# Kernel tuning notes

Measured on AMD Instinct MI355X. Metric: run time of the kernel, lower is better.

Reference implementation:

```python
import jax, jax.numpy as jnp
import numpy as np

B, T, N, H = 16, 49, 24, 256
S = 0.05  # init scale (keeps sigmoids/tanh out of saturation for numeric testing)


def setup_inputs() -> dict:
    key = jax.random.key(0)
    ks = jax.random.split(key, 16)
    rn = lambda k, shp: (jax.random.normal(k, shp, dtype=jnp.float32) * S)
    return dict(
        h=rn(ks[0], (B, T, N, H)),
        c_h=rn(ks[1], (B, T, N, H)),
        p=rn(ks[2], (B, T, N, H)),
        g_t=rn(ks[3], (B, T, N, H)),
        c_g_t=rn(ks[4], (B, T, N, H)),
        g_s=rn(ks[5], (B, T, N, H)),
        c_g_s=rn(ks[6], (B, T, N, H)),
        # 9 h-gates stacked in order: i, lt, ft, rt, s, gt, gs, o, c
        U=rn(ks[7], (9, N, H, H)),
        Wt=rn(ks[8], (9, N, 3 * H, H)),
        Ws=rn(ks[9], (9, N, H, H)),
        Zt=rn(ks[10], (9, N, H, H)),
        Zs=rn(ks[11], (9, N, H, H)),
        b=rn(ks[12], (9, N, 1, H)),
        # 6 global gates stacked in order: gtf, gtg, gto, gsf, gsg, gso
        Wg=rn(ks[13], (6, N, H, H)),
        Zg=rn(ks[14], (6, N, H, H)),
        bg=rn(ks[15], (6, N, 1, H)),
        train=1,
    )


def _cell(h, c_h, p, g_t, c_g_t, g_s, c_g_s, U, Wt, Ws, Zt, Zs, b, Wg, Zg, bg):
    pad_t = jnp.zeros_like(h[:, :, :1, :])
    pad_s = jnp.zeros_like(h[:, :1, :, :])
    # spatial (bone) neighbours along axis 2
    h_t_before = jnp.concatenate([pad_t, h[:, :, :-1, :]], axis=2)
    h_t_after = jnp.concatenate([h[:, :, 1:, :], pad_t], axis=2)
    h_tba = jnp.concatenate([h_t_before, h, h_t_after], axis=3)  # [B,T,N,3H]
    c_t_before = jnp.concatenate([pad_t, c_h[:, :, :-1, :]], axis=2)
    c_t_after = jnp.concatenate([c_h[:, :, 1:, :], pad_t], axis=2)
    # temporal predecessor along axis 1
    h_s_before = jnp.concatenate([pad_s, h[:, :-1, :, :]], axis=1)
    c_s_before = jnp.concatenate([pad_s, c_h[:, :-1, :, :]], axis=1)

    # Faithful quirk of the source: f_ft gate uses Zslt (the lt gate's Zs) for its g_s term.
    Zs_eff = Zs.at[2].set(Zs[1])

    # All 9 gate preactivations in one fused batched-GEMM pass: [9,B,T,N,H]
    pre = (jnp.einsum('btnh,gnhk->gbtnk', p, U)
           + jnp.einsum('btnm,gnmk->gbtnk', h_tba, Wt)
           + jnp.einsum('btnh,gnhk->gbtnk', h_s_before, Ws)
           + jnp.einsum('btnh,gnhk->gbtnk', g_t, Zt)
           + jnp.einsum('btnh,gnhk->gbtnk', g_s, Zs_eff)
           + b[:, None, None, :, 0, :])
    i_n, f_lt, f_ft, f_rt, f_s, f_gt, f_gs, o_n = jax.nn.sigmoid(pre[:8])
    c_n = jnp.tanh(pre[8])

    c_h_new = (f_lt * c_t_before + f_ft * c_h + f_rt * c_t_after
               + f_s * c_s_before + f_gt * c_g_t + f_gs * c_g_s + i_n * c_n)
    h_new = o_n * jnp.tanh(c_h_new)

    def _global(x_g, c_g, Wg3, Zg3, bg3):
        pre_g = (jnp.einsum('btnh,gnhk->gbtnk', h_new, Wg3)
                 + jnp.einsum('btnh,gnhk->gbtnk', x_g, Zg3)
                 + bg3[:, None, None, :, 0, :])
        f_g = jax.nn.sigmoid(pre_g[0])
        cand = jnp.tanh(pre_g[1])
        o_g = jax.nn.sigmoid(pre_g[2])
        c_g_new = f_g * c_g + (1.0 - f_g) * cand
        return o_g * jnp.tanh(c_g_new), c_g_new

    g_t_new, c_g_t_new = _global(g_t, c_g_t, Wg[:3], Zg[:3], bg[:3])
    g_s_new, c_g_s_new = _global(g_s, c_g_s, Wg[3:], Zg[3:], bg[3:])
    return h_new, c_h_new, g_t_new, c_g_t_new, g_s_new, c_g_s_new


def reference(h, c_h, p, g_t, c_g_t, g_s, c_g_s, U, Wt, Ws, Zt, Zs, b, Wg, Zg, bg, train):
    # `train` is a flag unused by the cell's math (kept for signature fidelity)
    return _cell(h, c_h, p, g_t, c_g_t, g_s, c_g_s, U, Wt, Ws, Zt, Zs, b, Wg, Zg, bg)
```

## Files before the change

kernel.cpp:

```cpp
#include <hip/hip_runtime.h>
#include <hip/hip_bf16.h>

typedef unsigned short u16;
typedef u16 u16x8 __attribute__((ext_vector_type(8)));
typedef short s16x8 __attribute__((ext_vector_type(8)));
typedef float f32x4 __attribute__((ext_vector_type(4)));
typedef unsigned int u32;

#define NN 24
#define TT 49
#define MR 784
#define SZT 4816896

__device__ inline u16 f2b(float f){
    __hip_bfloat16 b = __float2bfloat16(f); u16 r; __builtin_memcpy(&r, &b, 2); return r;
}
__device__ inline float sig_(float x){ return 1.f / (1.f + __expf(-x)); }
__device__ inline float tanh_(float x){ float e = __expf(2.f * x); return (e - 1.f) / (e + 1.f); }

__device__ inline void gld16(const u16* g, u16* l){
    __builtin_amdgcn_global_load_lds(
        (const __attribute__((address_space(1))) unsigned int*)g,
        (__attribute__((address_space(3))) unsigned int*)l, 16, 0, 0);
}

#define BAR()      __builtin_amdgcn_s_barrier()
#define WAITVM(N)  asm volatile("s_waitcnt vmcnt(" #N ")" ::: "memory")
#define WAITVL(N)  asm volatile("s_waitcnt vmcnt(" #N ") lgkmcnt(0)" ::: "memory")

#define WT0_ELEMS ((size_t)216 * 256 * 1792)
#define WT1_ELEMS ((size_t)144 * 256 * 512)

__global__ __launch_bounds__(256) void prep_all(
    const float* __restrict__ U,  const float* __restrict__ Wt,
    const float* __restrict__ Ws, const float* __restrict__ Zt,
    const float* __restrict__ Zs, const float* __restrict__ Wg,
    const float* __restrict__ Zg,
    const float* __restrict__ p,  const float* __restrict__ h,
    const float* __restrict__ g_t, const float* __restrict__ g_s,
    u16* __restrict__ wt0, u16* __restrict__ wt1, u16* __restrict__ Abf)
{
    __shared__ u16 T[64][72];
    const int tid = threadIdx.x;
    const int lin = blockIdx.x;

    if (lin < 24192) {
        const int kt = lin % 28, ct = (lin / 28) % 4, z = lin / 112;
        const int n = z % NN, g = z / NN;
        const int k0 = kt * 64;
        const float* wbase;
        if (k0 < 256)       wbase = U  + (size_t)((g * NN + n) * 256 + k0)          * 256;
        else if (k0 < 1024) wbase = Wt + (size_t)((g * NN + n) * 768 + (k0 - 256))  * 256;
        else if (k0 < 1280) wbase = Ws + (size_t)((g * NN + n) * 256 + (k0 - 1024)) * 256;
        else if (k0 < 1536) wbase = Zt + (size_t)((g * NN + n) * 256 + (k0 - 1280)) * 256;
        else { const int g2 = (g == 2) ? 1 : g;
               wbase = Zs + (size_t)((g2 * NN + n) * 256 + (k0 - 1536)) * 256; }
        const int colg = ct * 64 + (tid & 15) * 4;
        #pragma unroll
        for (int it = 0; it < 4; ++it) {
            const int krl = (tid >> 4) + it * 16;
            const float4 v = *(const float4*)(wbase + (size_t)krl * 256 + colg);
            const int cl = (tid & 15) * 4;
            T[cl + 0][krl] = f2b(v.x); T[cl + 1][krl] = f2b(v.y);
            T[cl + 2][krl] = f2b(v.z); T[cl + 3][krl] = f2b(v.w);
        }
        __syncthreads();
        const int col_l = tid >> 2, ks = (tid & 3) * 16;
        const int ktile = 2 * kt + (ks >> 5);
        const int koff  = ks & 31;
        u16* dst = wt0 + (size_t)z * 458752 + (size_t)ktile * 8192
                       + (size_t)(ct * 64 + col_l) * 32 + koff;
        u16x8 w0, w1;
        #pragma unroll
        for (int j2 = 0; j2 < 8; ++j2) { w0[j2] = T[col_l][ks + j2]; w1[j2] = T[col_l][ks + 8 + j2]; }
        *(u16x8*)(dst) = w0; *(u16x8*)(dst + 8) = w1;
    } else if (lin < 28800) {
        const int l = lin - 24192;
        const int kt = l % 8, ct = (l / 8) % 4, z = l / 32;
        const int k0 = kt * 64;
        const float* wbase = (k0 < 256)
            ? Wg + (size_t)(z * 256 + k0) * 256
            : Zg + (size_t)(z * 256 + (k0 - 256)) * 256;
        const int colg = ct * 64 + (tid & 15) * 4;
        #pragma unroll
        for (int it = 0; it < 4; ++it) {
            const int krl = (tid >> 4) + it * 16;
            const float4 v = *(const float4*)(wbase + (size_t)krl * 256 + colg);
            const int cl = (tid & 15) * 4;
            T[cl + 0][krl] = f2b(v.x); T[cl + 1][krl] = f2b(v.y);
            T[cl + 2][krl] = f2b(v.z); T[cl + 3][krl] = f2b(v.w);
        }
        __syncthreads();
        const int col_l = tid >> 2, ks = (tid & 3) * 16;
        const int ktile = 2 * kt + (ks >> 5);
        const int koff  = ks & 31;
        u16* dst = wt1 + (size_t)z * 131072 + (size_t)ktile * 8192
                       + (size_t)(ct * 64 + col_l) * 32 + koff;
        u16x8 w0, w1;
        #pragma unroll
        for (int j2 = 0; j2 < 8; ++j2) { w0[j2] = T[col_l][ks + j2]; w1[j2] = T[col_l][ks + 8 + j2]; }
        *(u16x8*)(dst) = w0; *(u16x8*)(dst + 8) = w1;
    } else {
        const int l = lin - 28800;
        const int bx = l % 13, kt = (l / 13) % 56, n = l / 728;
        const int row = bx * 64 + (tid >> 2);
        if (row >= MR) return;
        const int c  = tid & 3;
        const int kg = kt * 32 + c * 8;
        const int seg = kg >> 8, koff = kg & 255;
        const int ec = (row * NN + n) * 256 + koff;
        const float* src = nullptr; bool valid = true;
        switch (seg) {
            case 0: src = p + ec; break;
            case 1: valid = (n > 0);          src = h + ec - 256; break;
            case 2: src = h + ec; break;
            case 3: valid = (n < NN - 1);     src = h + ec + 256; break;
            case 4: valid = (row % TT) != 0;  src = h + ec - NN * 256; break;
            case 5: src = g_t + ec; break;
            default: src = g_s + ec; break;
        }
        float4 lo = {0.f,0.f,0.f,0.f}, hi = lo;
        if (valid) { lo = *(const float4*)src; hi = *(const float4*)(src + 4); }
        u16x8 w;
        w[0] = f2b(lo.x); w[1] = f2b(lo.y); w[2] = f2b(lo.z); w[3] = f2b(lo.w);
        w[4] = f2b(hi.x); w[5] = f2b(hi.y); w[6] = f2b(hi.z); w[7] = f2b(hi.w);
        *(u16x8*)(Abf + ((size_t)(n * 56 + kt) * MR + row) * 32 + c * 8) = w;
    }
}

#define AB8 4096
#define BB8 18432

__global__ __launch_bounds__(512, 1) void fused_cell8(
    const float* __restrict__ c_h, const float* __restrict__ c_g_t,
    const float* __restrict__ c_g_s,
    const u16* __restrict__ Abf, const u16* __restrict__ WT0,
    const float* __restrict__ Bias,
    float* __restrict__ h_new, float* __restrict__ c_h_new)
{
    extern __shared__ u16 smem[];

    const int tid = threadIdx.x;
    const int lin = blockIdx.x;
    const int xcd = lin & 7, j = lin >> 3;
    const int mtile = j % 7;
    const int slab  = (j / 7) * 8 + xcd;
    const int ntile = slab & 3, n = slab >> 2;

    const int wave = tid >> 6, lane = tid & 63;
    const int rh = wave >> 2, cq = wave & 3;
    const int lrow = lane & 15, lci = lane >> 4;

    const int rloc = wave * 16 + (lane >> 2);
    const int rglb = mtile * 128 + rloc;
    const int rsrc = (rglb < MR) ? rglb : (MR - 1);
    const int ach  = (lane & 3) ^ ((rloc >> 1) & 3);
    const u16* aSrc = Abf + ((size_t)(n * 56) * MR + rsrc) * 32 + ach * 8;
    const int aDst = wave * 512 + lane * 8;

    const int g0 = (wave < 4) ? wave * 5 : 20 + (wave - 4) * 4;
    const int ng = (wave < 4) ? 5 : 4;
    const u16* bSrc[5]; int bDst[5];
    #pragma unroll
    for (int i = 0; i < 5; ++i) {
        const int G = g0 + ((i < ng) ? i : 0);
        const int g = G >> 2, q = G & 3;
        const int c = q * 16 + (lane >> 2);
        const int ch = (lane & 3) ^ ((c >> 1) & 3);
        bSrc[i] = WT0 + (size_t)n * 458752 + (size_t)g * 11010048
                + (size_t)(ntile * 64 + c) * 32 + ch * 8;
        bDst[i] = g * 2048 + q * 512 + lane * 8;
    }

    int aro[4];
    #pragma unroll
    for (int m = 0; m < 4; ++m) {
        const int row = rh * 64 + m * 16 + lrow;
        aro[m] = row * 32 + ((lci ^ ((row >> 1) & 3)) << 3);
    }
    const int colr = cq * 16 + lrow;
    const int bro  = colr * 32 + ((lci ^ ((colr >> 1) & 3)) << 3);

    f32x4 acc[9][4];
    #pragma unroll
    for (int g = 0; g < 9; ++g)
        #pragma unroll
        for (int m = 0; m < 4; ++m) acc[g][m] = f32x4{0.f, 0.f, 0.f, 0.f};

    auto dma = [&](int kt, int buf) {
        gld16(aSrc + (size_t)kt * (MR * 32), &smem[buf * AB8 + aDst]);
        const size_t ko = (size_t)kt * 8192;
        u16* bBase = &smem[2 * AB8 + buf * BB8];
        #pragma unroll
        for (int i = 0; i < 5; ++i)
            if (i < ng) gld16(bSrc[i] + ko, bBase + bDst[i]);
    };
    auto publish = [&]() {
        if (wave < 4) { WAITVM(6); } else { WAITVM(5); }
        BAR();
    };
    auto domfma = [&](int buf) {
        const u16* Asb = smem + buf * AB8;
        const u16* Bsb = smem + 2 * AB8 + buf * BB8;
        s16x8 af[4];
        #pragma unroll
        for (int m = 0; m < 4; ++m) af[m] = *(const s16x8*)(&Asb[aro[m]]);
        __builtin_amdgcn_s_setprio(1);
        #pragma unroll
        for (int g = 0; g < 9; ++g) {
            const s16x8 bf = *(const s16x8*)(&Bsb[g * 2048 + bro]);
            #pragma unroll
            for (int m = 0; m < 4; ++m)
                acc[g][m] = __builtin_amdgcn_mfma_f32_16x16x32_bf16(af[m], bf, acc[g][m], 0, 0, 0);
        }
        __builtin_amdgcn_s_setprio(0);
    };

    dma(0, 0);
    WAITVM(0); BAR();
    dma(1, 1);
    for (int kt = 0; kt < 54; kt += 2) {
        domfma(0);
        BAR();
        dma(kt + 2, 0);
        publish();
        domfma(1);
        BAR();
        dma(kt + 3, 1);
        publish();
    }
    domfma(0);
    BAR();
    WAITVM(0); BAR();
    domfma(1);

    const int col = ntile * 64 + cq * 16 + lrow;
    float bv[9];
    #pragma unroll
    for (int g = 0; g < 9; ++g) bv[g] = Bias[(g * NN + n) * 256 + col];

    #pragma unroll
    for (int m = 0; m < 4; ++m) {
        #pragma unroll
        for (int i = 0; i < 4; ++i) {
            const int row = mtile * 128 + rh * 64 + m * 16 + (lane >> 4) * 4 + i;
            if (row < MR) {
                const size_t e = ((size_t)(row * NN + n)) * 256 + col;
                const float i_n  = sig_(acc[0][m][i] + bv[0]);
                const float f_lt = sig_(acc[1][m][i] + bv[1]);
                const float f_ft = sig_(acc[2][m][i] + bv[2]);
                const float f_rt = sig_(acc[3][m][i] + bv[3]);
                const float f_s  = sig_(acc[4][m][i] + bv[4]);
                const float f_gt = sig_(acc[5][m][i] + bv[5]);
                const float f_gs = sig_(acc[6][m][i] + bv[6]);
                const float o_n  = sig_(acc[7][m][i] + bv[7]);
                const float c_n  = tanh_(acc[8][m][i] + bv[8]);
                const float cb = (n > 0)      ? c_h[e - 256] : 0.f;
                const float ca = (n < NN - 1) ? c_h[e + 256] : 0.f;
                const float cs = (row % TT)   ? c_h[e - NN * 256] : 0.f;
                const float cn = f_lt * cb + f_ft * c_h[e] + f_rt * ca
                               + f_s * cs + f_gt * c_g_t[e] + f_gs * c_g_s[e]
                               + i_n * c_n;
                c_h_new[e] = cn;
                h_new[e]   = o_n * tanh_(cn);
            }
        }
    }
}

__global__ __launch_bounds__(256, 4) void fused_global5(
    const float* __restrict__ hn,   const float* __restrict__ g_t,
    const float* __restrict__ g_s,  const float* __restrict__ c_g_t,
    const float* __restrict__ c_g_s,
    const u16* __restrict__ WT1, const float* __restrict__ Bg,
    float* __restrict__ out2, float* __restrict__ out3,
    float* __restrict__ out4, float* __restrict__ out5)
{
    __shared__ u16 smem[2 * 2048 + 2 * 6144];

    const int tid = threadIdx.x;
    const int lin = blockIdx.x;
    const int xcd = lin & 7, j = lin >> 3;
    const int mtile = j % 13;
    const int slab  = (j / 13) * 8 + xcd;
    const int ntile = slab & 3;
    const int zz    = slab >> 2;
    const int n = zz % NN, grp = zz / NN;

    const float* xg = grp ? g_s : g_t;
    const float* cg = grp ? c_g_s : c_g_t;
    float* og  = grp ? out4 : out2;
    float* ocg = grp ? out5 : out3;

    const int s_r = tid >> 2, s_c = tid & 3;
    const int gr  = mtile * 64 + s_r;
    const bool mval = (gr < MR);
    const int ec = (gr * NN + n) * 256;

    const int wro = s_r * 32 + ((s_c ^ ((s_r >> 1) & 3)) << 3);

    const int wave = tid >> 6, lane = tid & 63;
    const int lrow = lane & 15, lci = lane >> 4;

    int aro[4];
    #pragma unroll
    for (int m = 0; m < 4; ++m) {
        const int row = m * 16 + lrow;
        aro[m] = row * 32 + ((lci ^ ((row >> 1) & 3)) << 3);
    }
    const int colr = wave * 16 + lrow;
    const int bro  = colr * 32 + ((lci ^ ((colr >> 1) & 3)) << 3);

    const u16* wbase = WT1 + (size_t)(grp * 3 * NN + n) * 131072
                           + (size_t)(ntile * 64) * 32 + wro;

    f32x4 acc[3][4];
    #pragma unroll
    for (int g = 0; g < 3; ++g)
        #pragma unroll
        for (int m = 0; m < 4; ++m) acc[g][m] = f32x4{0.f, 0.f, 0.f, 0.f};

    float4 aOlo, aOhi, aNlo, aNhi;

    auto loadA = [&](int kt, float4& lo, float4& hi) {
        const int K0 = kt * 32, koff = (K0 & 255) + s_c * 8;
        const float* src = ((K0 < 256) ? hn : xg) + ec + koff;
        lo = make_float4(0.f, 0.f, 0.f, 0.f); hi = lo;
        if (mval) { lo = *(const float4*)src; hi = *(const float4*)(src + 4); }
    };
    auto storeA = [&](int buf, const float4& lo, const float4& hi) {
        u16x8 aw;
        aw[0] = f2b(lo.x); aw[1] = f2b(lo.y); aw[2] = f2b(lo.z); aw[3] = f2b(lo.w);
        aw[4] = f2b(hi.x); aw[5] = f2b(hi.y); aw[6] = f2b(hi.z); aw[7] = f2b(hi.w);
        *(u16x8*)(&smem[buf * 2048 + wro]) = aw;
    };
    auto dmaB = [&](int kt, int buf) {
        const u16* wb = wbase + (size_t)kt * 8192;
        u16* dst = &smem[2 * 2048 + buf * 6144 + tid * 8];
        #pragma unroll
        for (int g = 0; g < 3; ++g)
            gld16(wb + (size_t)g * 3145728, dst + g * 2048);
    };
    auto domfma = [&](int buf) {
        const u16* Asb = smem + buf * 2048;
        const u16* Bsb = smem + 2 * 2048 + buf * 6144;
        s16x8 af[4];
        #pragma unroll
        for (int m = 0; m < 4; ++m) af[m] = *(const s16x8*)(&Asb[aro[m]]);
        __builtin_amdgcn_s_setprio(1);
        #pragma unroll
        for (int g = 0; g < 3; ++g) {
            const s16x8 bf = *(const s16x8*)(&Bsb[g * 2048 + bro]);
            #pragma unroll
            for (int m = 0; m < 4; ++m)
                acc[g][m] = __builtin_amdgcn_mfma_f32_16x16x32_bf16(af[m], bf, acc[g][m], 0, 0, 0);
        }
        __builtin_amdgcn_s_setprio(0);
    };

    loadA(0, aOlo, aOhi);
    dmaB(0, 0);
    storeA(0, aOlo, aOhi);
    loadA(1, aOlo, aOhi);
    dmaB(1, 1);
    WAITVL(5); BAR();
    for (int kt = 0; kt < 14; kt += 2) {
        domfma(0);
        BAR();
        loadA(kt + 2, aNlo, aNhi);
        dmaB(kt + 2, 0);
        storeA(1, aOlo, aOhi);
        WAITVL(5); BAR();
        domfma(1);
        BAR();
        loadA(kt + 3, aOlo, aOhi);
        dmaB(kt + 3, 1);
        storeA(0, aNlo, aNhi);
        WAITVL(5); BAR();
    }
    domfma(0);
    BAR();
    storeA(1, aOlo, aOhi);
    WAITVL(0); BAR();
    domfma(1);

    const int col = ntile * 64 + wave * 16 + lrow;
    float bv[3];
    #pragma unroll
    for (int g = 0; g < 3; ++g) bv[g] = Bg[((grp * 3 + g) * NN + n) * 256 + col];

    #pragma unroll
    for (int m = 0; m < 4; ++m) {
        #pragma unroll
        for (int i = 0; i < 4; ++i) {
            const int row = mtile * 64 + m * 16 + (lane >> 4) * 4 + i;
            if (row < MR) {
                const size_t e = ((size_t)(row * NN + n)) * 256 + col;
                const float f    = sig_(acc[0][m][i] + bv[0]);
                const float cand = tanh_(acc[1][m][i] + bv[1]);
                const float o    = sig_(acc[2][m][i] + bv[2]);
                const float cn = f * cg[e] + (1.f - f) * cand;
                ocg[e] = cn;
                og[e]  = o * tanh_(cn);
            }
        }
    }
}

extern "C" void kernel_launch(void* const* d_in, const int* in_sizes, int n_in,
                              void* d_out, int out_size, void* d_ws, size_t ws_size,
                              hipStream_t stream)
{
    const float* h     = (const float*)d_in[0];
    const float* c_h   = (const float*)d_in[1];
    const float* p     = (const float*)d_in[2];
    const float* g_t   = (const float*)d_in[3];
    const float* c_g_t = (const float*)d_in[4];
    const float* g_s   = (const float*)d_in[5];
    const float* c_g_s = (const float*)d_in[6];
    const float* U     = (const float*)d_in[7];
    const float* Wt    = (const float*)d_in[8];
    const float* Ws    = (const float*)d_in[9];
    const float* Zt    = (const float*)d_in[10];
    const float* Zs    = (const float*)d_in[11];
    const float* bb    = (const float*)d_in[12];
    const float* Wg    = (const float*)d_in[13];
    const float* Zg    = (const float*)d_in[14];
    const float* bg    = (const float*)d_in[15];

    float* out0 = (float*)d_out;
    float* out1 = out0 + (size_t)SZT;
    float* out2 = out1 + (size_t)SZT;
    float* out3 = out2 + (size_t)SZT;
    float* out4 = out3 + (size_t)SZT;
    float* out5 = out4 + (size_t)SZT;

    u16* wt0 = (u16*)d_ws;
    u16* wt1 = wt0 + WT0_ELEMS;
    u16* abf = wt1 + WT1_ELEMS;

    dim3 blk(256);
    prep_all<<<dim3(46272), blk, 0, stream>>>(U, Wt, Ws, Zt, Zs, Wg, Zg,
                                              p, h, g_t, g_s, wt0, wt1, abf);

    hipFuncSetAttribute((const void*)fused_cell8,
                        hipFuncAttributeMaxDynamicSharedMemorySize, 90112);
    fused_cell8<<<dim3(672), dim3(512), 90112, stream>>>(
        c_h, c_g_t, c_g_s, abf, wt0, bb, out0, out1);
    fused_global5<<<dim3(2496), blk, 0, stream>>>(
        out0, g_t, g_s, c_g_t, c_g_s, wt1, bg, out2, out3, out4, out5);
}
```

Baseline: 470.4 us.

## Triple-buffer the gate GEMM pipeline and shrink M tiles to exact 112 rows

Switches the fused cell kernel from a double-buffered LDS pipeline to a triple-buffered one, so the next tile's DMA is issued before the current MFMA work and only one barrier is needed per k-step. M tiles shrink from 128 to 112 rows, which divides the 784 rows exactly across the 7 tiles and removes padded, wasted MFMA work. The upper-half waves now do 3 instead of 4 row fragments, and B loads are interleaved across waves. The cost is a larger LDS footprint and some imbalance between the two wave halves.

```diff
diff --git a/kernel.cpp b/kernel.cpp
--- a/kernel.cpp
+++ b/kernel.cpp
@@ -128,10 +128,11 @@
     }
 }
 
-#define AB8 4096
-#define BB8 18432
-
-__global__ __launch_bounds__(512, 1) void fused_cell8(
+#define ABUF9 3584
+#define BBUF9 18432
+#define BUFE9 (ABUF9 + BBUF9)
+
+__global__ __launch_bounds__(512, 1) void fused_cell9(
     const float* __restrict__ c_h, const float* __restrict__ c_g_t,
     const float* __restrict__ c_g_s,
     const u16* __restrict__ Abf, const u16* __restrict__ WT0,
@@ -142,34 +143,32 @@
 
     const int tid = threadIdx.x;
     const int lin = blockIdx.x;
-    const int xcd = lin & 7, j = lin >> 3;
-    const int mtile = j % 7;
-    const int slab  = (j / 7) * 8 + xcd;
+    const int xcd = lin & 7, jj = lin >> 3;
+    const int mtile = jj % 7;
+    const int slab  = (jj / 7) * 8 + xcd;
     const int ntile = slab & 3, n = slab >> 2;
 
     const int wave = tid >> 6, lane = tid & 63;
     const int rh = wave >> 2, cq = wave & 3;
     const int lrow = lane & 15, lci = lane >> 4;
-
-    const int rloc = wave * 16 + (lane >> 2);
-    const int rglb = mtile * 128 + rloc;
-    const int rsrc = (rglb < MR) ? rglb : (MR - 1);
+    const int MC = (rh == 0) ? 4 : 3;
+
+    const int rloc = (wave < 7) ? (wave * 16 + (lane >> 2)) : 0;
     const int ach  = (lane & 3) ^ ((rloc >> 1) & 3);
-    const u16* aSrc = Abf + ((size_t)(n * 56) * MR + rsrc) * 32 + ach * 8;
+    const u16* aSrc = Abf + ((size_t)(n * 56) * MR + mtile * 112 + rloc) * 32 + ach * 8;
     const int aDst = wave * 512 + lane * 8;
 
-    const int g0 = (wave < 4) ? wave * 5 : 20 + (wave - 4) * 4;
     const int ng = (wave < 4) ? 5 : 4;
     const u16* bSrc[5]; int bDst[5];
     #pragma unroll
     for (int i = 0; i < 5; ++i) {
-        const int G = g0 + ((i < ng) ? i : 0);
+        const int G = (i < ng) ? (wave + 8 * i) : 0;
         const int g = G >> 2, q = G & 3;
         const int c = q * 16 + (lane >> 2);
         const int ch = (lane & 3) ^ ((c >> 1) & 3);
         bSrc[i] = WT0 + (size_t)n * 458752 + (size_t)g * 11010048
                 + (size_t)(ntile * 64 + c) * 32 + ch * 8;
-        bDst[i] = g * 2048 + q * 512 + lane * 8;
+        bDst[i] = ABUF9 + g * 2048 + q * 512 + lane * 8;
     }
 
     int aro[4];
@@ -179,7 +178,7 @@
         aro[m] = row * 32 + ((lci ^ ((row >> 1) & 3)) << 3);
     }
     const int colr = cq * 16 + lrow;
-    const int bro  = colr * 32 + ((lci ^ ((colr >> 1) & 3)) << 3);
+    const int bro  = ABUF9 + colr * 32 + ((lci ^ ((colr >> 1) & 3)) << 3);
 
     f32x4 acc[9][4];
     #pragma unroll
@@ -188,49 +187,44 @@
         for (int m = 0; m < 4; ++m) acc[g][m] = f32x4{0.f, 0.f, 0.f, 0.f};
 
     auto dma = [&](int kt, int buf) {
-        gld16(aSrc + (size_t)kt * (MR * 32), &smem[buf * AB8 + aDst]);
+        u16* base = smem + buf * BUFE9;
+        if (wave < 7) gld16(aSrc + (size_t)kt * (MR * 32), base + aDst);
         const size_t ko = (size_t)kt * 8192;
-        u16* bBase = &smem[2 * AB8 + buf * BB8];
         #pragma unroll
         for (int i = 0; i < 5; ++i)
-            if (i < ng) gld16(bSrc[i] + ko, bBase + bDst[i]);
-    };
-    auto publish = [&]() {
-        if (wave < 4) { WAITVM(6); } else { WAITVM(5); }
-        BAR();
+            if (i < ng) gld16(bSrc[i] + ko, base + bDst[i]);
+    };
+    auto waitw = [&]() {
+        if (wave < 4)      { WAITVM(6); }
+        else if (wave < 7) { WAITVM(5); }
+        else               { WAITVM(4); }
     };
     auto domfma = [&](int buf) {
-        const u16* Asb = smem + buf * AB8;
-        const u16* Bsb = smem + 2 * AB8 + buf * BB8;
+        const u16* base = smem + buf * BUFE9;
         s16x8 af[4];
         #pragma unroll
-        for (int m = 0; m < 4; ++m) af[m] = *(const s16x8*)(&Asb[aro[m]]);
+        for (int m = 0; m < 4; ++m)
+            if (m < MC) af[m] = *(const s16x8*)(&base[aro[m]]);
         __builtin_amdgcn_s_setprio(1);
         #pragma unroll
         for (int g = 0; g < 9; ++g) {
-            const s16x8 bf = *(const s16x8*)(&Bsb[g * 2048 + bro]);
+            const s16x8 bf = *(const s16x8*)(&base[g * 2048 + bro]);
             #pragma unroll
             for (int m = 0; m < 4; ++m)
-                acc[g][m] = __builtin_amdgcn_mfma_f32_16x16x32_bf16(af[m], bf, acc[g][m], 0, 0, 0);
+                if (m < MC)
+                    acc[g][m] = __builtin_amdgcn_mfma_f32_16x16x32_bf16(af[m], bf, acc[g][m], 0, 0, 0);
         }
         __builtin_amdgcn_s_setprio(0);
     };
 
-    dma(0, 0);
-    WAITVM(0); BAR();
-    dma(1, 1);
-    for (int kt = 0; kt < 54; kt += 2) {
-        domfma(0);
-        BAR();
-        dma(kt + 2, 0);
-        publish();
-        domfma(1);
-        BAR();
-        dma(kt + 3, 1);
-        publish();
+    dma(0, 0); dma(1, 1);
+    waitw(); BAR();
+    for (int t3 = 0; t3 < 54; t3 += 3) {
+        dma(t3 + 2, 2); domfma(0); waitw(); BAR();
+        dma(t3 + 3, 0); domfma(1); waitw(); BAR();
+        dma(t3 + 4, 1); domfma(2); waitw(); BAR();
     }
     domfma(0);
-    BAR();
     WAITVM(0); BAR();
     domfma(1);
 
@@ -241,10 +235,10 @@
 
     #pragma unroll
     for (int m = 0; m < 4; ++m) {
-        #pragma unroll
-        for (int i = 0; i < 4; ++i) {
-            const int row = mtile * 128 + rh * 64 + m * 16 + (lane >> 4) * 4 + i;
-            if (row < MR) {
+        if (m < MC) {
+            #pragma unroll
+            for (int i = 0; i < 4; ++i) {
+                const int row = mtile * 112 + rh * 64 + m * 16 + (lane >> 4) * 4 + i;
                 const size_t e = ((size_t)(row * NN + n)) * 256 + col;
                 const float i_n  = sig_(acc[0][m][i] + bv[0]);
                 const float f_lt = sig_(acc[1][m][i] + bv[1]);
@@ -443,9 +437,10 @@
     prep_all<<<dim3(46272), blk, 0, stream>>>(U, Wt, Ws, Zt, Zs, Wg, Zg,
                                               p, h, g_t, g_s, wt0, wt1, abf);
 
-    hipFuncSetAttribute((const void*)fused_cell8,
-                        hipFuncAttributeMaxDynamicSharedMemorySize, 90112);
-    fused_cell8<<<dim3(672), dim3(512), 90112, stream>>>(
+    const int ldsBytes = 3 * BUFE9 * (int)sizeof(u16);
+    hipFuncSetAttribute((const void*)fused_cell9,
+                        hipFuncAttributeMaxDynamicSharedMemorySize, ldsBytes);
+    fused_cell9<<<dim3(672), dim3(512), ldsBytes, stream>>>(
         c_h, c_g_t, c_g_s, abf, wt0, bb, out0, out1);
     fused_global5<<<dim3(2496), blk, 0, stream>>>(
         out0, g_t, g_s, c_g_t, c_g_s, wt1, bg, out2, out3, out4, out5);
```

Result: faster. 452.5 us (-3.8%).
